# Optimization experiments

Hardware: AMD Instinct MI355X
Metric: run time of the kernel (lower is better)

Reference implementation:

```python
import jax, jax.numpy as jnp
import numpy as np

HEADS = 8
DIM_HEAD = 64  # note: per-head dim is inner_dim/heads = 512 due to the module's inner_dim = dim_head*dim
SCALE = DIM_HEAD ** (-0.5)
EPS = 1e-5


def layernorm(x, gamma):
    # nn.LayerNorm(dim, elementwise_affine=False) then x * (gamma + 1)
    mu = jnp.mean(x, axis=-1, keepdims=True)
    var = jnp.var(x, axis=-1, keepdims=True)
    xn = (x - mu) * jax.lax.rsqrt(var + EPS)
    return xn * (gamma + 1.0)


def setup_inputs() -> dict:
    key = jax.random.key(0)
    ks = jax.random.split(key, 6)
    b, n, dim = 2, 2048, 256
    inner = DIM_HEAD * dim  # 4096
    x = jax.random.normal(ks[0], (b, n, dim), dtype=jnp.float32)
    gamma = jax.random.normal(ks[1], (dim,), dtype=jnp.float32) * 0.02
    Wq = jax.random.normal(ks[2], (inner, dim), dtype=jnp.float32) * 0.02
    Wk = jax.random.normal(ks[3], (inner, dim), dtype=jnp.float32) * 0.02
    Wv = jax.random.normal(ks[4], (inner, dim), dtype=jnp.float32) * 0.02
    Wo = jax.random.normal(ks[5], (dim, inner), dtype=jnp.float32) * 0.02
    return {"x": x, "gamma": gamma, "Wq": Wq, "Wk": Wk, "Wv": Wv, "Wo": Wo}


def reference(x, gamma, Wq, Wk, Wv, Wo):
    b, n, dim = x.shape
    h = HEADS
    xn = layernorm(x, gamma)  # reuse_attention=True -> norm = LayerNorm(dim)
    # self-attention: context = xn (cross_attend=False, norm_context=Identity)
    q = jnp.einsum('bnd,ed->bne', xn, Wq).reshape(b, n, h, -1).transpose(0, 2, 1, 3)
    k = jnp.einsum('bnd,ed->bne', xn, Wk).reshape(b, n, h, -1).transpose(0, 2, 1, 3)
    v = jnp.einsum('bnd,ed->bne', xn, Wv).reshape(b, n, h, -1).transpose(0, 2, 1, 3)
    qk_sim = jnp.einsum('bhqd,bhkd->bhqk', q * SCALE, k)
    attn = jax.nn.softmax(qk_sim, axis=-1)  # dropout p=0.0 -> identity
    dot = jnp.einsum('bhqk,bhkd->bhqd', attn, v)
    out = dot.transpose(0, 2, 1, 3).reshape(b, n, -1)
    out = jnp.einsum('bne,de->bnd', out, Wo)
    return out
```

## Files before the change

### kernel.cpp

```cpp
#include <hip/hip_runtime.h>


typedef unsigned short u16;
typedef unsigned int u32;
typedef __bf16 bf16x8 __attribute__((ext_vector_type(8)));
typedef float f32x4 __attribute__((ext_vector_type(4)));

__device__ __forceinline__ u16 f2bf(float f) {
    u32 u = __builtin_bit_cast(u32, f);
    u += 0x7fffu + ((u >> 16) & 1u);
    return (u16)(u >> 16);
}

#define GLDS16(G, L)                                                                  \
    __builtin_amdgcn_global_load_lds((const __attribute__((address_space(1))) u32*)(G), \
                                     (__attribute__((address_space(3))) u32*)(L), 16, 0, 0)

template <int N> __device__ __forceinline__ void vm_wait() {
    asm volatile("s_waitcnt vmcnt(%0)" :: "n"(N) : "memory");
}
__device__ __forceinline__ void lgk0() {
    asm volatile("s_waitcnt lgkmcnt(0)" ::: "memory");
}
__device__ __forceinline__ void bar() {
    __builtin_amdgcn_s_barrier();
    __builtin_amdgcn_sched_barrier(0);
}

template <typename OutT, bool ATOMIC>
__global__ void __launch_bounds__(256, 3) gemm_bt(
    const u16* __restrict__ A, const u16* __restrict__ B, OutT* __restrict__ C,
    int K, int lda, int ldb, int ldc,
    long sAh, long sAb, long sBh, long sBb, long sCh, long sCb,
    int H, int NB, long ksA, long ksB)
{
    __shared__ u16 ldsA[3][128 * 32];
    __shared__ u16 ldsB[3][128 * 32];

    const int z = blockIdx.z;
    const int zh = z % H;
    const int zq = z / H;
    const int zb = zq % NB;
    const int kc = zq / NB;
    A += (size_t)zh * sAh + (size_t)zb * sAb + (size_t)kc * ksA;
    B += (size_t)zh * sBh + (size_t)zb * sBb + (size_t)kc * ksB;
    C += (size_t)zh * sCh + (size_t)zb * sCb;

    const int bm = blockIdx.y * 128;
    const int bn = blockIdx.x * 128;
    const int t = threadIdx.x;
    const int w = t >> 6, l = t & 63;
    const int wm = w >> 1, wn = w & 1;
    const int lr = l & 15, lk = l >> 4;
    const int sw = lk ^ ((lr >> 1) & 3);

    const int m0 = t >> 2, s0 = t & 3;
    const int c0 = s0 ^ ((m0 >> 1) & 3);
    const int m1 = 64 + m0;
    const int c1 = s0 ^ ((m1 >> 1) & 3);
    const int o0 = (t & ~63) * 8;
    const int o1 = (256 + (t & ~63)) * 8;

    const u16* gA0 = A + (size_t)(bm + m0) * lda + c0 * 8;
    const u16* gA1 = A + (size_t)(bm + m1) * lda + c1 * 8;
    const u16* gB0 = B + (size_t)(bn + m0) * ldb + c0 * 8;
    const u16* gB1 = B + (size_t)(bn + m1) * ldb + c1 * 8;

    f32x4 acc[4][4];
#pragma unroll
    for (int i = 0; i < 4; ++i)
#pragma unroll
        for (int j = 0; j < 4; ++j)
            acc[i][j] = f32x4{0.f, 0.f, 0.f, 0.f};

    const int nk = K >> 5;

    GLDS16(gA0, &ldsA[0][o0]); GLDS16(gA1, &ldsA[0][o1]);
    GLDS16(gB0, &ldsB[0][o0]); GLDS16(gB1, &ldsB[0][o1]);
    gA0 += 32; gA1 += 32; gB0 += 32; gB1 += 32;
    GLDS16(gA0, &ldsA[1][o0]); GLDS16(gA1, &ldsA[1][o1]);
    GLDS16(gB0, &ldsB[1][o0]); GLDS16(gB1, &ldsB[1][o1]);
    gA0 += 32; gA1 += 32; gB0 += 32; gB1 += 32;

    int cur = 0, wsl = 2;
    for (int kt = 0; kt < nk - 1; ++kt) {
        vm_wait<4>(); bar();
        if (kt + 2 < nk) {
            GLDS16(gA0, &ldsA[wsl][o0]); GLDS16(gA1, &ldsA[wsl][o1]);
            GLDS16(gB0, &ldsB[wsl][o0]); GLDS16(gB1, &ldsB[wsl][o1]);
            gA0 += 32; gA1 += 32; gB0 += 32; gB1 += 32;
        }
        bf16x8 av[4], bv[4];
#pragma unroll
        for (int i = 0; i < 4; ++i) {
            av[i] = *(const bf16x8*)&ldsA[cur][(wm * 64 + i * 16 + lr) * 32 + sw * 8];
            bv[i] = *(const bf16x8*)&ldsB[cur][(wn * 64 + i * 16 + lr) * 32 + sw * 8];
        }
        __builtin_amdgcn_s_setprio(1);
#pragma unroll
        for (int i = 0; i < 4; ++i)
#pragma unroll
            for (int j = 0; j < 4; ++j)
                acc[i][j] = __builtin_amdgcn_mfma_f32_16x16x32_bf16(av[i], bv[j], acc[i][j], 0, 0, 0);
        __builtin_amdgcn_s_setprio(0);
        cur = (cur == 2) ? 0 : cur + 1;
        wsl = (wsl == 2) ? 0 : wsl + 1;
    }
    vm_wait<0>(); bar();
    {
        bf16x8 av[4], bv[4];
#pragma unroll
        for (int i = 0; i < 4; ++i) {
            av[i] = *(const bf16x8*)&ldsA[cur][(wm * 64 + i * 16 + lr) * 32 + sw * 8];
            bv[i] = *(const bf16x8*)&ldsB[cur][(wn * 64 + i * 16 + lr) * 32 + sw * 8];
        }
        __builtin_amdgcn_s_setprio(1);
#pragma unroll
        for (int i = 0; i < 4; ++i)
#pragma unroll
            for (int j = 0; j < 4; ++j)
                acc[i][j] = __builtin_amdgcn_mfma_f32_16x16x32_bf16(av[i], bv[j], acc[i][j], 0, 0, 0);
        __builtin_amdgcn_s_setprio(0);
    }

#pragma unroll
    for (int i = 0; i < 4; ++i) {
        const int row0 = bm + wm * 64 + i * 16 + lk * 4;
#pragma unroll
        for (int j = 0; j < 4; ++j) {
            const int col = bn + wn * 64 + j * 16 + lr;
#pragma unroll
            for (int r = 0; r < 4; ++r) {
                const size_t idx = (size_t)(row0 + r) * ldc + col;
                const float v = acc[i][j][r];
                if constexpr (ATOMIC) {
                    atomicAdd(&C[idx], v);
                } else if constexpr (sizeof(OutT) == 2) {
                    C[idx] = (OutT)f2bf(v);
                } else {
                    C[idx] = (OutT)v;
                }
            }
        }
    }
}

__global__ void __launch_bounds__(256, 2) attn_fused(
    const u16* __restrict__ Y, const u16* __restrict__ xn,
    const u16* __restrict__ Zt, float* __restrict__ opart)
{
    __shared__ u16 ldsB[3][128 * 32];
    __shared__ u16 ldsZ[2][256 * 32];
    __shared__ u16 Pl[64 * 136];
    __shared__ float l_lds[64];

    const int wgid = blockIdx.x + 32 * blockIdx.y;
    const int xcd = wgid & 7;
    const int p = wgid >> 3;
    const int hb = 2 * xcd + (p & 1);
    const int i0 = (p >> 1) * 64;
    const int h = hb >> 1, b = hb & 1;

    const int t = threadIdx.x;
    const int w = t >> 6, l = t & 63;
    const int wm = w >> 1, wn = w & 1;
    const int lr = l & 15, lk = l >> 4;
    const int sw = lk ^ ((lr >> 1) & 3);

    if (t < 64) l_lds[t] = 0.f;

    const u16* Yb = Y + (size_t)(b * 2048 + i0) * 2048 + h * 256;
    const u16* xb = xn + (size_t)b * 2048 * 256;
    const u16* Zb = Zt + (size_t)b * 4194304 + (size_t)h * 524288;

    const int m0 = t >> 2, s0 = t & 3;
    const int c0 = s0 ^ ((m0 >> 1) & 3);
    const int m1 = 64 + m0;
    const int c1 = s0 ^ ((m1 >> 1) & 3);
    const int oB0 = (t & ~63) * 8;
    const int oB1 = (256 + (t & ~63)) * 8;

    const u16 *gZ0, *gZ1, *gZ2, *gZ3;
    const int oZ0 = (t & ~63) * 8;
    const int oZ1 = (256 + (t & ~63)) * 8;
    const int oZ2 = (512 + (t & ~63)) * 8;
    const int oZ3 = (768 + (t & ~63)) * 8;
    {
        const int q0 = t, q1 = 256 + t, q2 = 512 + t, q3 = 768 + t;
        const int mz0 = q0 >> 2, mz1 = q1 >> 2, mz2 = q2 >> 2, mz3 = q3 >> 2;
        const int cz0 = (q0 & 3) ^ ((mz0 >> 1) & 3);
        const int cz1 = (q1 & 3) ^ ((mz1 >> 1) & 3);
        const int cz2 = (q2 & 3) ^ ((mz2 >> 1) & 3);
        const int cz3 = (q3 & 3) ^ ((mz3 >> 1) & 3);
        gZ0 = Zb + (size_t)mz0 * 2048 + cz0 * 8;
        gZ1 = Zb + (size_t)mz1 * 2048 + cz1 * 8;
        gZ2 = Zb + (size_t)mz2 * 2048 + cz2 * 8;
        gZ3 = Zb + (size_t)mz3 * 2048 + cz3 * 8;
    }

    u16* ldsY = &ldsZ[0][0];
#pragma unroll
    for (int pp = 0; pp < 8; ++pp) {
        const int q = pp * 256 + t;
        const int kt = q >> 8, qq = q & 255;
        const int m = qq >> 2, s = qq & 3;
        const int c = s ^ ((m >> 1) & 3);
        GLDS16(Yb + (size_t)m * 2048 + kt * 32 + c * 8,
               &ldsY[(pp * 256 + (t & ~63)) * 8]);
    }
    GLDS16(xb + (size_t)m0 * 256 + c0 * 8, &ldsB[0][oB0]);
    GLDS16(xb + (size_t)m1 * 256 + c1 * 8, &ldsB[0][oB1]);
    GLDS16(xb + (size_t)m0 * 256 + 32 + c0 * 8, &ldsB[1][oB0]);
    GLDS16(xb + (size_t)m1 * 256 + 32 + c1 * 8, &ldsB[1][oB1]);
    vm_wait<4>();
    bar();

    bf16x8 yr[8][2];
#pragma unroll
    for (int kt = 0; kt < 8; ++kt)
#pragma unroll
        for (int i = 0; i < 2; ++i)
            yr[kt][i] = *(const bf16x8*)&ldsY[kt * 2048 + (wm * 32 + i * 16 + lr) * 32 + sw * 8];

    f32x4 acc_o[2][8];
#pragma unroll
    for (int i = 0; i < 2; ++i)
#pragma unroll
        for (int j = 0; j < 8; ++j)
            acc_o[i][j] = f32x4{0.f, 0.f, 0.f, 0.f};
    float lsum[8];
#pragma unroll
    for (int i = 0; i < 8; ++i) lsum[i] = 0.f;

#define S_STEP(KT, VMC, ISSUE)                                                        \
    {                                                                                 \
        vm_wait<VMC>(); bar();                                                        \
        ISSUE;                                                                        \
        bf16x8 bv[4];                                                                 \
        _Pragma("unroll")                                                             \
        for (int j = 0; j < 4; ++j)                                                   \
            bv[j] = *(const bf16x8*)&ldsB[(KT) % 3][(wn * 64 + j * 16 + lr) * 32 + sw * 8]; \
        __builtin_amdgcn_s_setprio(1);                                                \
        _Pragma("unroll")                                                             \
        for (int j = 0; j < 4; ++j) {                                                 \
            acc_s[0][j] = __builtin_amdgcn_mfma_f32_16x16x32_bf16(yr[KT][0], bv[j], acc_s[0][j], 0, 0, 0); \
            acc_s[1][j] = __builtin_amdgcn_mfma_f32_16x16x32_bf16(yr[KT][1], bv[j], acc_s[1][j], 0, 0, 0); \
        }                                                                             \
        __builtin_amdgcn_s_setprio(0);                                                \
    }

#define PV_STEP(KT, VMC, ISSUE)                                                       \
    {                                                                                 \
        vm_wait<VMC>(); bar();                                                        \
        ISSUE;                                                                        \
        bf16x8 av[2];                                                                 \
        av[0] = *(const bf16x8*)&Pl[(wm * 32 + lr) * 136 + (KT) * 32 + lk * 8];       \
        av[1] = *(const bf16x8*)&Pl[(wm * 32 + 16 + lr) * 136 + (KT) * 32 + lk * 8];  \
        __builtin_amdgcn_s_setprio(1);                                                \
        _Pragma("unroll")                                                             \
        for (int jf = 0; jf < 8; ++jf) {                                              \
            const bf16x8 bz = *(const bf16x8*)&ldsZ[(KT) & 1][(wn * 128 + jf * 16 + lr) * 32 + sw * 8]; \
            acc_o[0][jf] = __builtin_amdgcn_mfma_f32_16x16x32_bf16(av[0], bz, acc_o[0][jf], 0, 0, 0);   \
            acc_o[1][jf] = __builtin_amdgcn_mfma_f32_16x16x32_bf16(av[1], bz, acc_o[1][jf], 0, 0, 0);   \
        }                                                                             \
        __builtin_amdgcn_s_setprio(0);                                                \
    }

#define ISSUE_B(JBASE, KK, SLOT)                                                      \
    GLDS16(JBASE + (size_t)m0 * 256 + (KK) * 32 + c0 * 8, &ldsB[SLOT][oB0]);          \
    GLDS16(JBASE + (size_t)m1 * 256 + (KK) * 32 + c1 * 8, &ldsB[SLOT][oB1])

#define ISSUE_Z(OFF, ZBUF)                                                            \
    GLDS16(gZ0 + (OFF), &ldsZ[ZBUF][oZ0]);                                            \
    GLDS16(gZ1 + (OFF), &ldsZ[ZBUF][oZ1]);                                            \
    GLDS16(gZ2 + (OFF), &ldsZ[ZBUF][oZ2]);                                            \
    GLDS16(gZ3 + (OFF), &ldsZ[ZBUF][oZ3])

    for (int jt = 0; jt < 16; ++jt) {
        const int j0 = jt * 128;
        const int jn = ((jt + 1) & 15) * 128;
        const u16* xbj = xb + (size_t)j0 * 256;
        const u16* xbn = xb + (size_t)jn * 256;

        f32x4 acc_s[2][4];
#pragma unroll
        for (int i = 0; i < 2; ++i)
#pragma unroll
            for (int j = 0; j < 4; ++j)
                acc_s[i][j] = f32x4{0.f, 0.f, 0.f, 0.f};

        S_STEP(0, 2, ISSUE_B(xbj, 2, 2))
        S_STEP(1, 2, ISSUE_B(xbj, 3, 0))
        S_STEP(2, 2, ISSUE_B(xbj, 4, 1))
        S_STEP(3, 2, ISSUE_B(xbj, 5, 2))
        S_STEP(4, 2, ISSUE_B(xbj, 6, 0))
        S_STEP(5, 2, ISSUE_B(xbj, 7, 1))
        S_STEP(6, 2, ISSUE_Z(j0, 0))
        S_STEP(7, 4, ISSUE_Z(j0 + 32, 1))

#pragma unroll
        for (int i = 0; i < 2; ++i)
#pragma unroll
            for (int j = 0; j < 4; ++j)
#pragma unroll
                for (int r = 0; r < 4; ++r) {
                    const float e = __expf(acc_s[i][j][r]);
                    lsum[i * 4 + r] += e;
                    Pl[(wm * 32 + i * 16 + lk * 4 + r) * 136 + wn * 64 + j * 16 + lr] = f2bf(e);
                }
        lgk0();

        PV_STEP(0, 4, ((void)0))
        PV_STEP(1, 0, ISSUE_Z(j0 + 64, 0))
        PV_STEP(2, 0, ISSUE_Z(j0 + 96, 1); ISSUE_B(xbn, 0, 0))
        PV_STEP(3, 2, ISSUE_B(xbn, 1, 1))
    }

#pragma unroll
    for (int i = 0; i < 2; ++i)
#pragma unroll
        for (int r = 0; r < 4; ++r) {
            float s = lsum[i * 4 + r];
            s += __shfl_xor(s, 1, 64);
            s += __shfl_xor(s, 2, 64);
            s += __shfl_xor(s, 4, 64);
            s += __shfl_xor(s, 8, 64);
            if (lr == 0) atomicAdd(&l_lds[wm * 32 + i * 16 + lk * 4 + r], s);
        }
    __syncthreads();

    float* oh = opart + (size_t)h * 1048576;
#pragma unroll
    for (int i = 0; i < 2; ++i)
#pragma unroll
        for (int r = 0; r < 4; ++r) {
            const int row = wm * 32 + i * 16 + lk * 4 + r;
            const float rl = 1.0f / l_lds[row];
            float* orow = oh + (size_t)(b * 2048 + i0 + row) * 256 + wn * 128;
#pragma unroll
            for (int jf = 0; jf < 8; ++jf)
                orow[jf * 16 + lr] = acc_o[i][jf][r] * rl;
        }
}

__global__ void __launch_bounds__(256) hreduce_kernel(const float* __restrict__ opart,
                                                      float* __restrict__ out)
{
    const size_t i = (size_t)blockIdx.x * 256 + threadIdx.x;
    float4 s = ((const float4*)opart)[i];
#pragma unroll
    for (int h = 1; h < 8; ++h) {
        const float4 v = ((const float4*)(opart + (size_t)h * 1048576))[i];
        s.x += v.x; s.y += v.y; s.z += v.z; s.w += v.w;
    }
    ((float4*)out)[i] = s;
}

__global__ void __launch_bounds__(256) tcast3_kernel(const float* __restrict__ Wq,
                                                     const float* __restrict__ Wk,
                                                     const float* __restrict__ Wv,
                                                     u16* __restrict__ dst)
{
    __shared__ u16 tile[64][66];
    const int z = blockIdx.z;
    const int wsel = z >> 3, h = z & 7;
    const float* src = (wsel == 0) ? Wq : (wsel == 1) ? Wk : Wv;
    const float scale = (wsel == 0) ? 0.125f : 1.0f;
    u16* d = dst + (size_t)wsel * 4194304;
    const int d0 = blockIdx.x * 64;
    const int a0 = blockIdx.y * 64;
    const int t = threadIdx.x;
    const int c = t & 63, r0 = t >> 6;
#pragma unroll
    for (int rr = 0; rr < 16; ++rr) {
        const int r = r0 + rr * 4;
        tile[r][c] = f2bf(src[((size_t)h * 2048 + d0 + r) * 256 + a0 + c] * scale);
    }
    __syncthreads();
#pragma unroll
    for (int rr = 0; rr < 16; ++rr) {
        const int r = r0 + rr * 4;
        d[((size_t)h * 256 + a0 + r) * 2048 + d0 + c] = tile[c][r];
    }
}

__global__ void __launch_bounds__(64) ln_kernel(const float* __restrict__ x,
                                                const float* __restrict__ g,
                                                u16* __restrict__ xn)
{
    const size_t row = blockIdx.x;
    const int l = threadIdx.x;
    const float4 v = ((const float4*)(x + row * 256))[l];
    float s = v.x + v.y + v.z + v.w;
    float q = v.x * v.x + v.y * v.y + v.z * v.z + v.w * v.w;
#pragma unroll
    for (int o = 32; o > 0; o >>= 1) {
        s += __shfl_xor(s, o, 64);
        q += __shfl_xor(q, o, 64);
    }
    const float mu = s * (1.0f / 256.0f);
    const float var = q * (1.0f / 256.0f) - mu * mu;
    const float rs = rsqrtf(var + 1e-5f);
    const float4 gg = ((const float4*)g)[l];
    ushort4 o4;
    o4.x = f2bf((v.x - mu) * rs * (gg.x + 1.0f));
    o4.y = f2bf((v.y - mu) * rs * (gg.y + 1.0f));
    o4.z = f2bf((v.z - mu) * rs * (gg.z + 1.0f));
    o4.w = f2bf((v.w - mu) * rs * (gg.w + 1.0f));
    ((ushort4*)(xn + row * 256))[l] = o4;
}

__global__ void __launch_bounds__(256) cast_bf16_kernel(const float* __restrict__ src,
                                                        u16* __restrict__ dst, float scale)
{
    const size_t i = (size_t)blockIdx.x * 256 + threadIdx.x;
    const float4 v = ((const float4*)src)[i];
    ushort4 o4;
    o4.x = f2bf(v.x * scale);
    o4.y = f2bf(v.y * scale);
    o4.z = f2bf(v.z * scale);
    o4.w = f2bf(v.w * scale);
    ((ushort4*)dst)[i] = o4;
}

extern "C" void kernel_launch(void* const* d_in, const int* in_sizes, int n_in,
                              void* d_out, int out_size, void* d_ws, size_t ws_size,
                              hipStream_t stream)
{
    (void)in_sizes; (void)n_in; (void)ws_size; (void)out_size;
    const float* x     = (const float*)d_in[0];
    const float* gamma = (const float*)d_in[1];
    const float* Wq    = (const float*)d_in[2];
    const float* Wk    = (const float*)d_in[3];
    const float* Wv    = (const float*)d_in[4];
    const float* Wo    = (const float*)d_in[5];
    float* out = (float*)d_out;

    char* ws = (char*)d_ws;
    const size_t MB = 1048576;
    u16* wqt   = (u16*)(ws);
    u16* wkt   = (u16*)(ws + 8 * MB);
    u16* wvt   = (u16*)(ws + 16 * MB);
    u16* wo    = (u16*)(ws + 24 * MB);
    u16* xn    = (u16*)(ws + 32 * MB);
    u16* Mt    = (u16*)(ws + 34 * MB);
    u16* Nb    = (u16*)(ws + 35 * MB);
    float* MtF = (float*)(ws + 36 * MB);
    float* NbF = (float*)(ws + 38 * MB);
    u16* Y     = (u16*)(ws + 44 * MB);
    u16* Zt    = (u16*)(ws + 60 * MB);
    float* opart = (float*)(ws);

    hipMemsetAsync(MtF, 0, 4 * MB, stream);

    tcast3_kernel<<<dim3(32, 4, 24), 256, 0, stream>>>(Wq, Wk, Wv, wqt);
    cast_bf16_kernel<<<4096, 256, 0, stream>>>(Wo, wo, 1.0f);
    ln_kernel<<<4096, 64, 0, stream>>>(x, gamma, xn);

    gemm_bt<float, true><<<dim3(2, 2, 32), 256, 0, stream>>>(
        wkt, wqt, MtF, 512, 2048, 2048, 256,
        524288L, 0, 524288L, 0, 65536L, 0, 8, 1, 512L, 512L);

    gemm_bt<float, true><<<dim3(2, 2, 32), 256, 0, stream>>>(
        wo, wvt, NbF, 512, 16384, 2048, 256,
        2048L, 0, 524288L, 0, 65536L, 0, 8, 1, 512L, 512L);

    cast_bf16_kernel<<<1024, 256, 0, stream>>>(MtF, Mt, 1.0f);

    gemm_bt<u16, false><<<dim3(16, 32, 1), 256, 0, stream>>>(
        xn, Mt, Y, 256, 256, 256, 2048,
        0, 0, 0, 0, 0, 0, 1, 1, 0, 0);

    gemm_bt<u16, false><<<dim3(16, 16, 2), 256, 0, stream>>>(
        Nb, xn, Zt, 256, 256, 256, 2048,
        0, 0, 0, 524288L, 0, 4194304L, 1, 2, 0, 0);

    attn_fused<<<dim3(32, 16), 256, 0, stream>>>(Y, xn, Zt, opart);

    hreduce_kernel<<<1024, 256, 0, stream>>>(opart, out);
}
```

Baseline: 276.0 us.

## Load xn operand straight to registers and quad-buffer Z tiles in LDS

Result: slower. 419.4 us (+51.9%).

```diff
diff --git a/kernel.cpp b/kernel.cpp
--- a/kernel.cpp
+++ b/kernel.cpp
@@ -149,10 +149,8 @@
     const u16* __restrict__ Y, const u16* __restrict__ xn,
     const u16* __restrict__ Zt, float* __restrict__ opart)
 {
-    __shared__ u16 ldsB[3][128 * 32];
-    __shared__ u16 ldsZ[2][256 * 32];
-    __shared__ u16 Pl[64 * 136];
-    __shared__ float l_lds[64];
+    __shared__ u16 ldsZ[4][8192];
+    __shared__ u16 Pl[8192];
 
     const int wgid = blockIdx.x + 32 * blockIdx.y;
     const int xcd = wgid & 7;
@@ -167,18 +165,9 @@
     const int lr = l & 15, lk = l >> 4;
     const int sw = lk ^ ((lr >> 1) & 3);
 
-    if (t < 64) l_lds[t] = 0.f;
-
     const u16* Yb = Y + (size_t)(b * 2048 + i0) * 2048 + h * 256;
     const u16* xb = xn + (size_t)b * 2048 * 256;
     const u16* Zb = Zt + (size_t)b * 4194304 + (size_t)h * 524288;
-
-    const int m0 = t >> 2, s0 = t & 3;
-    const int c0 = s0 ^ ((m0 >> 1) & 3);
-    const int m1 = 64 + m0;
-    const int c1 = s0 ^ ((m1 >> 1) & 3);
-    const int oB0 = (t & ~63) * 8;
-    const int oB1 = (256 + (t & ~63)) * 8;
 
     const u16 *gZ0, *gZ1, *gZ2, *gZ3;
     const int oZ0 = (t & ~63) * 8;
@@ -208,11 +197,7 @@
         GLDS16(Yb + (size_t)m * 2048 + kt * 32 + c * 8,
                &ldsY[(pp * 256 + (t & ~63)) * 8]);
     }
-    GLDS16(xb + (size_t)m0 * 256 + c0 * 8, &ldsB[0][oB0]);
-    GLDS16(xb + (size_t)m1 * 256 + c1 * 8, &ldsB[0][oB1]);
-    GLDS16(xb + (size_t)m0 * 256 + 32 + c0 * 8, &ldsB[1][oB0]);
-    GLDS16(xb + (size_t)m1 * 256 + 32 + c1 * 8, &ldsB[1][oB1]);
-    vm_wait<4>();
+    vm_wait<0>();
     bar();
 
     bf16x8 yr[8][2];
@@ -221,6 +206,8 @@
 #pragma unroll
         for (int i = 0; i < 2; ++i)
             yr[kt][i] = *(const bf16x8*)&ldsY[kt * 2048 + (wm * 32 + i * 16 + lr) * 32 + sw * 8];
+    lgk0();
+    bar();
 
     f32x4 acc_o[2][8];
 #pragma unroll
@@ -232,55 +219,19 @@
 #pragma unroll
     for (int i = 0; i < 8; ++i) lsum[i] = 0.f;
 
-#define S_STEP(KT, VMC, ISSUE)                                                        \
-    {                                                                                 \
-        vm_wait<VMC>(); bar();                                                        \
-        ISSUE;                                                                        \
-        bf16x8 bv[4];                                                                 \
-        _Pragma("unroll")                                                             \
-        for (int j = 0; j < 4; ++j)                                                   \
-            bv[j] = *(const bf16x8*)&ldsB[(KT) % 3][(wn * 64 + j * 16 + lr) * 32 + sw * 8]; \
-        __builtin_amdgcn_s_setprio(1);                                                \
-        _Pragma("unroll")                                                             \
-        for (int j = 0; j < 4; ++j) {                                                 \
-            acc_s[0][j] = __builtin_amdgcn_mfma_f32_16x16x32_bf16(yr[KT][0], bv[j], acc_s[0][j], 0, 0, 0); \
-            acc_s[1][j] = __builtin_amdgcn_mfma_f32_16x16x32_bf16(yr[KT][1], bv[j], acc_s[1][j], 0, 0, 0); \
-        }                                                                             \
-        __builtin_amdgcn_s_setprio(0);                                                \
-    }
-
-#define PV_STEP(KT, VMC, ISSUE)                                                       \
-    {                                                                                 \
-        vm_wait<VMC>(); bar();                                                        \
-        ISSUE;                                                                        \
-        bf16x8 av[2];                                                                 \
-        av[0] = *(const bf16x8*)&Pl[(wm * 32 + lr) * 136 + (KT) * 32 + lk * 8];       \
-        av[1] = *(const bf16x8*)&Pl[(wm * 32 + 16 + lr) * 136 + (KT) * 32 + lk * 8];  \
-        __builtin_amdgcn_s_setprio(1);                                                \
-        _Pragma("unroll")                                                             \
-        for (int jf = 0; jf < 8; ++jf) {                                              \
-            const bf16x8 bz = *(const bf16x8*)&ldsZ[(KT) & 1][(wn * 128 + jf * 16 + lr) * 32 + sw * 8]; \
-            acc_o[0][jf] = __builtin_amdgcn_mfma_f32_16x16x32_bf16(av[0], bz, acc_o[0][jf], 0, 0, 0);   \
-            acc_o[1][jf] = __builtin_amdgcn_mfma_f32_16x16x32_bf16(av[1], bz, acc_o[1][jf], 0, 0, 0);   \
-        }                                                                             \
-        __builtin_amdgcn_s_setprio(0);                                                \
-    }
-
-#define ISSUE_B(JBASE, KK, SLOT)                                                      \
-    GLDS16(JBASE + (size_t)m0 * 256 + (KK) * 32 + c0 * 8, &ldsB[SLOT][oB0]);          \
-    GLDS16(JBASE + (size_t)m1 * 256 + (KK) * 32 + c1 * 8, &ldsB[SLOT][oB1])
-
-#define ISSUE_Z(OFF, ZBUF)                                                            \
-    GLDS16(gZ0 + (OFF), &ldsZ[ZBUF][oZ0]);                                            \
-    GLDS16(gZ1 + (OFF), &ldsZ[ZBUF][oZ1]);                                            \
-    GLDS16(gZ2 + (OFF), &ldsZ[ZBUF][oZ2]);                                            \
-    GLDS16(gZ3 + (OFF), &ldsZ[ZBUF][oZ3])
+#define BFRAG(SRC, KK, J) \
+    (*(const bf16x8*)((SRC) + (size_t)(wn * 64 + (J) * 16 + lr) * 256 + (KK) * 32 + lk * 8))
+
+    bf16x8 bcur[4], bnxt[4];
+#pragma unroll
+    for (int j = 0; j < 4; ++j) bcur[j] = BFRAG(xb, 0, j);
+#pragma unroll
+    for (int j = 0; j < 4; ++j) bnxt[j] = BFRAG(xb, 1, j);
 
     for (int jt = 0; jt < 16; ++jt) {
         const int j0 = jt * 128;
-        const int jn = ((jt + 1) & 15) * 128;
         const u16* xbj = xb + (size_t)j0 * 256;
-        const u16* xbn = xb + (size_t)jn * 256;
+        const u16* xbn = xb + (size_t)(((jt + 1) & 15) * 128) * 256;
 
         f32x4 acc_s[2][4];
 #pragma unroll
@@ -289,14 +240,30 @@
             for (int j = 0; j < 4; ++j)
                 acc_s[i][j] = f32x4{0.f, 0.f, 0.f, 0.f};
 
-        S_STEP(0, 2, ISSUE_B(xbj, 2, 2))
-        S_STEP(1, 2, ISSUE_B(xbj, 3, 0))
-        S_STEP(2, 2, ISSUE_B(xbj, 4, 1))
-        S_STEP(3, 2, ISSUE_B(xbj, 5, 2))
-        S_STEP(4, 2, ISSUE_B(xbj, 6, 0))
-        S_STEP(5, 2, ISSUE_B(xbj, 7, 1))
-        S_STEP(6, 2, ISSUE_Z(j0, 0))
-        S_STEP(7, 4, ISSUE_Z(j0 + 32, 1))
+#pragma unroll
+        for (int kt = 0; kt < 8; ++kt) {
+            bf16x8 bnx2[4];
+            const u16* src = (kt < 6) ? xbj : xbn;
+            const int kk = (kt < 6) ? (kt + 2) : (kt - 6);
+#pragma unroll
+            for (int j = 0; j < 4; ++j) bnx2[j] = BFRAG(src, kk, j);
+            if (kt >= 4) {
+                const int zi = kt - 4;
+                GLDS16(gZ0 + j0 + zi * 32, &ldsZ[zi][oZ0]);
+                GLDS16(gZ1 + j0 + zi * 32, &ldsZ[zi][oZ1]);
+                GLDS16(gZ2 + j0 + zi * 32, &ldsZ[zi][oZ2]);
+                GLDS16(gZ3 + j0 + zi * 32, &ldsZ[zi][oZ3]);
+            }
+            __builtin_amdgcn_s_setprio(1);
+#pragma unroll
+            for (int j = 0; j < 4; ++j) {
+                acc_s[0][j] = __builtin_amdgcn_mfma_f32_16x16x32_bf16(yr[kt][0], bcur[j], acc_s[0][j], 0, 0, 0);
+                acc_s[1][j] = __builtin_amdgcn_mfma_f32_16x16x32_bf16(yr[kt][1], bcur[j], acc_s[1][j], 0, 0, 0);
+            }
+            __builtin_amdgcn_s_setprio(0);
+#pragma unroll
+            for (int j = 0; j < 4; ++j) { bcur[j] = bnxt[j]; bnxt[j] = bnx2[j]; }
+        }
 
 #pragma unroll
         for (int i = 0; i < 2; ++i)
@@ -304,18 +271,37 @@
             for (int j = 0; j < 4; ++j)
 #pragma unroll
                 for (int r = 0; r < 4; ++r) {
+                    const int row = wm * 32 + i * 16 + lk * 4 + r;
+                    const int col = wn * 64 + j * 16 + lr;
                     const float e = __expf(acc_s[i][j][r]);
                     lsum[i * 4 + r] += e;
-                    Pl[(wm * 32 + i * 16 + lk * 4 + r) * 136 + wn * 64 + j * 16 + lr] = f2bf(e);
+                    Pl[row * 128 + (col ^ ((row & 7) * 8))] = f2bf(e);
                 }
         lgk0();
-
-        PV_STEP(0, 4, ((void)0))
-        PV_STEP(1, 0, ISSUE_Z(j0 + 64, 0))
-        PV_STEP(2, 0, ISSUE_Z(j0 + 96, 1); ISSUE_B(xbn, 0, 0))
-        PV_STEP(3, 2, ISSUE_B(xbn, 1, 1))
-    }
-
+        vm_wait<0>();
+        bar();
+
+#pragma unroll
+        for (int kt = 0; kt < 4; ++kt) {
+            const int swz = (lr & 7) * 8;
+            bf16x8 av0 = *(const bf16x8*)&Pl[(wm * 32 + lr) * 128 + ((kt * 32 + lk * 8) ^ swz)];
+            bf16x8 av1 = *(const bf16x8*)&Pl[(wm * 32 + 16 + lr) * 128 + ((kt * 32 + lk * 8) ^ swz)];
+            __builtin_amdgcn_s_setprio(1);
+#pragma unroll
+            for (int jf = 0; jf < 8; ++jf) {
+                const bf16x8 bz = *(const bf16x8*)&ldsZ[kt][(wn * 128 + jf * 16 + lr) * 32 + sw * 8];
+                acc_o[0][jf] = __builtin_amdgcn_mfma_f32_16x16x32_bf16(av0, bz, acc_o[0][jf], 0, 0, 0);
+                acc_o[1][jf] = __builtin_amdgcn_mfma_f32_16x16x32_bf16(av1, bz, acc_o[1][jf], 0, 0, 0);
+            }
+            __builtin_amdgcn_s_setprio(0);
+            __builtin_amdgcn_sched_barrier(0);
+        }
+        bar();
+    }
+
+    float* l_lds = (float*)Pl;
+    if (t < 64) l_lds[t] = 0.f;
+    __syncthreads();
 #pragma unroll
     for (int i = 0; i < 2; ++i)
 #pragma unroll
```

## Merge preprocessing and paired GEMM launches into fewer combined kernels

Applied to the files above, without the earlier changes.

Result: faster. 253.8 us (-8.0%).

```diff
diff --git a/kernel.cpp b/kernel.cpp
--- a/kernel.cpp
+++ b/kernel.cpp
@@ -28,23 +28,12 @@
 }
 
 template <typename OutT, bool ATOMIC>
-__global__ void __launch_bounds__(256, 3) gemm_bt(
+__device__ __forceinline__ void gemm_core(
     const u16* __restrict__ A, const u16* __restrict__ B, OutT* __restrict__ C,
-    int K, int lda, int ldb, int ldc,
-    long sAh, long sAb, long sBh, long sBb, long sCh, long sCb,
-    int H, int NB, long ksA, long ksB)
+    int K, int lda, int ldb, int ldc)
 {
     __shared__ u16 ldsA[3][128 * 32];
     __shared__ u16 ldsB[3][128 * 32];
-
-    const int z = blockIdx.z;
-    const int zh = z % H;
-    const int zq = z / H;
-    const int zb = zq % NB;
-    const int kc = zq / NB;
-    A += (size_t)zh * sAh + (size_t)zb * sAb + (size_t)kc * ksA;
-    B += (size_t)zh * sBh + (size_t)zb * sBb + (size_t)kc * ksB;
-    C += (size_t)zh * sCh + (size_t)zb * sCb;
 
     const int bm = blockIdx.y * 128;
     const int bn = blockIdx.x * 128;
@@ -142,6 +131,111 @@
                 }
             }
         }
+    }
+}
+
+__global__ void __launch_bounds__(256, 3) gemm_w(
+    const u16* __restrict__ wkt, const u16* __restrict__ wqt,
+    const u16* __restrict__ wo, const u16* __restrict__ wvt,
+    float* __restrict__ MtF)
+{
+    const int z = blockIdx.z;
+    const int zh = z & 7;
+    const int q = z >> 3;
+    const int which = q & 1;
+    const int kc = q >> 1;
+    const u16* A; const u16* B; float* C; int lda;
+    if (which == 0) {
+        A = wkt + (size_t)zh * 524288 + kc * 512; lda = 2048;
+        B = wqt + (size_t)zh * 524288 + kc * 512;
+        C = MtF + (size_t)zh * 65536;
+    } else {
+        A = wo + (size_t)zh * 2048 + kc * 512;    lda = 16384;
+        B = wvt + (size_t)zh * 524288 + kc * 512;
+        C = MtF + 524288 + (size_t)zh * 65536;
+    }
+    gemm_core<float, true>(A, B, C, 512, lda, 2048, 256);
+}
+
+__global__ void __launch_bounds__(256, 3) gemm_yz(
+    const u16* __restrict__ xn, const u16* __restrict__ Mt,
+    const u16* __restrict__ Nb, u16* __restrict__ Y, u16* __restrict__ Zt)
+{
+    const int z = blockIdx.z;
+    const u16* A; const u16* B; u16* C;
+    if (z < 2) {
+        A = xn + (size_t)z * 524288;
+        B = Mt;
+        C = Y + (size_t)z * 4194304;
+    } else {
+        const int b = z - 2;
+        A = Nb;
+        B = xn + (size_t)b * 524288;
+        C = Zt + (size_t)b * 4194304;
+    }
+    gemm_core<u16, false>(A, B, C, 256, 256, 256, 2048);
+}
+
+__global__ void __launch_bounds__(256) prep_kernel(
+    const float* __restrict__ x, const float* __restrict__ g,
+    const float* __restrict__ Wq, const float* __restrict__ Wk,
+    const float* __restrict__ Wv, const float* __restrict__ Wo,
+    u16* __restrict__ wqkv, u16* __restrict__ wo_b,
+    u16* __restrict__ xn, float* __restrict__ MtF)
+{
+    __shared__ u16 tile[64][66];
+    const int bid = blockIdx.x;
+    const int t = threadIdx.x;
+    if (bid < 3072) {
+        const int bx = bid & 31, by = (bid >> 5) & 3, z = bid >> 7;
+        const int wsel = z >> 3, h = z & 7;
+        const float* src = (wsel == 0) ? Wq : (wsel == 1) ? Wk : Wv;
+        const float scale = (wsel == 0) ? 0.125f : 1.0f;
+        u16* d = wqkv + (size_t)wsel * 4194304;
+        const int d0 = bx * 64;
+        const int a0 = by * 64;
+        const int c = t & 63, r0 = t >> 6;
+#pragma unroll
+        for (int rr = 0; rr < 16; ++rr) {
+            const int r = r0 + rr * 4;
+            tile[r][c] = f2bf(src[((size_t)h * 2048 + d0 + r) * 256 + a0 + c] * scale);
+        }
+        __syncthreads();
+#pragma unroll
+        for (int rr = 0; rr < 16; ++rr) {
+            const int r = r0 + rr * 4;
+            d[((size_t)h * 256 + a0 + r) * 2048 + d0 + c] = tile[c][r];
+        }
+    } else if (bid < 7168) {
+        const size_t i = (size_t)(bid - 3072) * 256 + t;
+        const float4 v = ((const float4*)Wo)[i];
+        ushort4 o4;
+        o4.x = f2bf(v.x); o4.y = f2bf(v.y); o4.z = f2bf(v.z); o4.w = f2bf(v.w);
+        ((ushort4*)wo_b)[i] = o4;
+    } else if (bid < 8192) {
+        const size_t row = (size_t)(bid - 7168) * 4 + (t >> 6);
+        const int l = t & 63;
+        const float4 v = ((const float4*)(x + row * 256))[l];
+        float s = v.x + v.y + v.z + v.w;
+        float qq = v.x * v.x + v.y * v.y + v.z * v.z + v.w * v.w;
+#pragma unroll
+        for (int o = 32; o > 0; o >>= 1) {
+            s += __shfl_xor(s, o, 64);
+            qq += __shfl_xor(qq, o, 64);
+        }
+        const float mu = s * (1.0f / 256.0f);
+        const float var = qq * (1.0f / 256.0f) - mu * mu;
+        const float rs = rsqrtf(var + 1e-5f);
+        const float4 gg = ((const float4*)g)[l];
+        ushort4 o4;
+        o4.x = f2bf((v.x - mu) * rs * (gg.x + 1.0f));
+        o4.y = f2bf((v.y - mu) * rs * (gg.y + 1.0f));
+        o4.z = f2bf((v.z - mu) * rs * (gg.z + 1.0f));
+        o4.w = f2bf((v.w - mu) * rs * (gg.w + 1.0f));
+        ((ushort4*)(xn + row * 256))[l] = o4;
+    } else {
+        const size_t i = (size_t)(bid - 8192) * 256 + t;
+        ((float4*)MtF)[i] = float4{0.f, 0.f, 0.f, 0.f};
     }
 }
 
@@ -356,60 +450,6 @@
     ((float4*)out)[i] = s;
 }
 
-__global__ void __launch_bounds__(256) tcast3_kernel(const float* __restrict__ Wq,
-                                                     const float* __restrict__ Wk,
-                                                     const float* __restrict__ Wv,
-                                                     u16* __restrict__ dst)
-{
-    __shared__ u16 tile[64][66];
-    const int z = blockIdx.z;
-    const int wsel = z >> 3, h = z & 7;
-    const float* src = (wsel == 0) ? Wq : (wsel == 1) ? Wk : Wv;
-    const float scale = (wsel == 0) ? 0.125f : 1.0f;
-    u16* d = dst + (size_t)wsel * 4194304;
-    const int d0 = blockIdx.x * 64;
-    const int a0 = blockIdx.y * 64;
-    const int t = threadIdx.x;
-    const int c = t & 63, r0 = t >> 6;
-#pragma unroll
-    for (int rr = 0; rr < 16; ++rr) {
-        const int r = r0 + rr * 4;
-        tile[r][c] = f2bf(src[((size_t)h * 2048 + d0 + r) * 256 + a0 + c] * scale);
-    }
-    __syncthreads();
-#pragma unroll
-    for (int rr = 0; rr < 16; ++rr) {
-        const int r = r0 + rr * 4;
-        d[((size_t)h * 256 + a0 + r) * 2048 + d0 + c] = tile[c][r];
-    }
-}
-
-__global__ void __launch_bounds__(64) ln_kernel(const float* __restrict__ x,
-                                                const float* __restrict__ g,
-                                                u16* __restrict__ xn)
-{
-    const size_t row = blockIdx.x;
-    const int l = threadIdx.x;
-    const float4 v = ((const float4*)(x + row * 256))[l];
-    float s = v.x + v.y + v.z + v.w;
-    float q = v.x * v.x + v.y * v.y + v.z * v.z + v.w * v.w;
-#pragma unroll
-    for (int o = 32; o > 0; o >>= 1) {
-        s += __shfl_xor(s, o, 64);
-        q += __shfl_xor(q, o, 64);
-    }
-    const float mu = s * (1.0f / 256.0f);
-    const float var = q * (1.0f / 256.0f) - mu * mu;
-    const float rs = rsqrtf(var + 1e-5f);
-    const float4 gg = ((const float4*)g)[l];
-    ushort4 o4;
-    o4.x = f2bf((v.x - mu) * rs * (gg.x + 1.0f));
-    o4.y = f2bf((v.y - mu) * rs * (gg.y + 1.0f));
-    o4.z = f2bf((v.z - mu) * rs * (gg.z + 1.0f));
-    o4.w = f2bf((v.w - mu) * rs * (gg.w + 1.0f));
-    ((ushort4*)(xn + row * 256))[l] = o4;
-}
-
 __global__ void __launch_bounds__(256) cast_bf16_kernel(const float* __restrict__ src,
                                                         u16* __restrict__ dst, float scale)
 {
@@ -444,36 +484,19 @@
     u16* wo    = (u16*)(ws + 24 * MB);
     u16* xn    = (u16*)(ws + 32 * MB);
     u16* Mt    = (u16*)(ws + 34 * MB);
+    float* MtF = (float*)(ws + 36 * MB);
     u16* Nb    = (u16*)(ws + 35 * MB);
-    float* MtF = (float*)(ws + 36 * MB);
-    float* NbF = (float*)(ws + 38 * MB);
     u16* Y     = (u16*)(ws + 44 * MB);
     u16* Zt    = (u16*)(ws + 60 * MB);
     float* opart = (float*)(ws);
 
-    hipMemsetAsync(MtF, 0, 4 * MB, stream);
-
-    tcast3_kernel<<<dim3(32, 4, 24), 256, 0, stream>>>(Wq, Wk, Wv, wqt);
-    cast_bf16_kernel<<<4096, 256, 0, stream>>>(Wo, wo, 1.0f);
-    ln_kernel<<<4096, 64, 0, stream>>>(x, gamma, xn);
-
-    gemm_bt<float, true><<<dim3(2, 2, 32), 256, 0, stream>>>(
-        wkt, wqt, MtF, 512, 2048, 2048, 256,
-        524288L, 0, 524288L, 0, 65536L, 0, 8, 1, 512L, 512L);
-
-    gemm_bt<float, true><<<dim3(2, 2, 32), 256, 0, stream>>>(
-        wo, wvt, NbF, 512, 16384, 2048, 256,
-        2048L, 0, 524288L, 0, 65536L, 0, 8, 1, 512L, 512L);
+    prep_kernel<<<9216, 256, 0, stream>>>(x, gamma, Wq, Wk, Wv, Wo, wqt, wo, xn, MtF);
+
+    gemm_w<<<dim3(2, 2, 64), 256, 0, stream>>>(wkt, wqt, wo, wvt, MtF);
 
     cast_bf16_kernel<<<1024, 256, 0, stream>>>(MtF, Mt, 1.0f);
 
-    gemm_bt<u16, false><<<dim3(16, 32, 1), 256, 0, stream>>>(
-        xn, Mt, Y, 256, 256, 256, 2048,
-        0, 0, 0, 0, 0, 0, 1, 1, 0, 0);
-
-    gemm_bt<u16, false><<<dim3(16, 16, 2), 256, 0, stream>>>(
-        Nb, xn, Zt, 256, 256, 256, 2048,
-        0, 0, 0, 524288L, 0, 4194304L, 1, 2, 0, 0);
+    gemm_yz<<<dim3(16, 16, 4), 256, 0, stream>>>(xn, Mt, Nb, Y, Zt);
 
     attn_fused<<<dim3(32, 16), 256, 0, stream>>>(Y, xn, Zt, opart);
 
```
